# Kernel tuning notes

Measured on AMD Instinct MI355X. Metric: run time of the kernel, lower is better.

The kernel has to match this reference:

```python
import jax, jax.numpy as jnp
import numpy as np

B, S = 128, 512          # batch, padded expression length
D = 256                  # kos/identifier embedding dim (asserted equal)
KIND_D = 8               # token-kind embedding dim
EXPR_D = 512             # expression_encoding_dim
KOS_VOCAB = 256
KIND_VOCAB = 8
NUM_IDS = 8192
PAD_IDX = 0              # padding_idx -> zero embedding row
IDENTIFIER_KIND = 3
KOS_KINDS = (4, 5, 6)    # OPERATOR, SEPARATOR, KEYWORD


def setup_inputs() -> dict:
    key = jax.random.key(0)
    ks = jax.random.split(key, 8)
    token_type = jax.random.randint(ks[0], (B, S), 0, KIND_VOCAB, dtype=jnp.int32)
    kos_token_index = jax.random.randint(ks[1], (B * S,), 0, KOS_VOCAB, dtype=jnp.int32)
    identifier_indices = jax.random.randint(ks[2], (B * S,), 0, NUM_IDS, dtype=jnp.int32)
    encoded_identifiers = jax.random.normal(ks[3], (NUM_IDS, D), jnp.float32)
    kind_emb = jax.random.normal(ks[4], (KIND_VOCAB, KIND_D), jnp.float32).at[PAD_IDX].set(0.0)
    kos_emb = jax.random.normal(ks[5], (KOS_VOCAB, D), jnp.float32).at[PAD_IDX].set(0.0)
    sp = 1.0 / np.sqrt(KIND_D + D)
    W_proj = jax.random.uniform(ks[6], (KIND_D + D, EXPR_D), jnp.float32, -sp, sp)
    b_proj = jnp.zeros((EXPR_D,), jnp.float32)
    sa = 1.0 / np.sqrt(EXPR_D)
    W_add = jax.random.uniform(ks[7], (EXPR_D, EXPR_D), jnp.float32, -sa, sa)
    b_add = jnp.zeros((EXPR_D,), jnp.float32)
    return {
        'token_type': token_type,
        'kos_token_index': kos_token_index,
        'identifier_indices': identifier_indices,
        'encoded_identifiers': encoded_identifiers,
        'kind_emb': kind_emb,
        'kos_emb': kos_emb,
        'W_proj': W_proj,
        'b_proj': b_proj,
        'W_add': W_add,
        'b_add': b_add,
    }


def reference(token_type, kos_token_index, identifier_indices, encoded_identifiers,
              kind_emb, kos_emb, W_proj, b_proj, W_add, b_add):
    # token-kind embedding lookup: [B, S, KIND_D]
    kind_e = kind_emb[token_type]

    flat_kind = token_type.reshape(-1)                       # [B*S]
    is_id = flat_kind == IDENTIFIER_KIND
    is_kos = (flat_kind == KOS_KINDS[0]) | (flat_kind == KOS_KINDS[1]) | (flat_kind == KOS_KINDS[2])

    # embedding-table gathers (sources for masked_scatter, consumed in order)
    id_src = encoded_identifiers[identifier_indices]         # [B*S, D]
    kos_src = kos_emb[kos_token_index]                       # [B*S, D]

    # masked_scatter semantics: the k-th True position gets the k-th source row
    rank_id = jnp.maximum(jnp.cumsum(is_id) - 1, 0)
    rank_kos = jnp.maximum(jnp.cumsum(is_kos) - 1, 0)
    enc = jnp.where(is_id[:, None], id_src[rank_id], jnp.float32(0.0))
    enc = jnp.where(is_kos[:, None], kos_src[rank_kos], enc)
    enc = enc.reshape(B, S, D)

    # concat + 2-layer MLP (dropout is identity in eval mode)
    x = jnp.concatenate([kind_e, enc], axis=-1)              # [B, S, KIND_D + D]
    x = jax.nn.relu(x @ W_proj + b_proj)                     # [B, S, EXPR_D]
    x = jax.nn.relu(x @ W_add + b_add)                       # [B, S, EXPR_D]
    return x
```

## Files before the change

### kernel.cpp

```cpp
#include <hip/hip_runtime.h>
#include <hip/hip_bf16.h>

#define BB 128
#define SS 512
#define NPOS (BB*SS)
#define DD 256
#define KIND_D 8
#define EXPR_D 512
#define KOS_VOCAB 256
#define NUM_IDS 8192
#define IDENTIFIER_KIND 3
#define TROWS 9088

typedef unsigned short u16;
typedef __attribute__((ext_vector_type(8))) short s16x8;
typedef __attribute__((ext_vector_type(8))) unsigned short u16x8;
typedef __attribute__((ext_vector_type(4))) float f32x4;

__device__ __forceinline__ u16 bf16bits(float v) {
    __hip_bfloat16 h = __float2bfloat16(v);
    return *(u16*)&h;
}
__device__ __forceinline__ float bf16tof(u16 b) {
    __hip_bfloat16 h = *(__hip_bfloat16*)&b;
    return __bfloat162float(h);
}

__global__ __launch_bounds__(256) void prep_kernel(const float* __restrict__ W2,
                                                   const float* __restrict__ kind_emb,
                                                   const float* __restrict__ Wp,
                                                   const float* __restrict__ bp,
                                                   const int* __restrict__ token_type,
                                                   u16* __restrict__ Wt,
                                                   u16* __restrict__ Wt1,
                                                   float* __restrict__ kindc,
                                                   int2* __restrict__ blkcnt) {
    __shared__ float tile[32][33];
    __shared__ int swid[4], swkos[4];
    const int bi = blockIdx.x;
    const int t = threadIdx.x;

    if (bi < 256) {
        const int n0 = (bi & 15) * 32;
        const int k0 = (bi >> 4) * 32;
        const int lj = t & 31, li = t >> 5;
        #pragma unroll
        for (int p = 0; p < 4; ++p) {
            int i = li + p * 8;
            tile[i][lj] = W2[(size_t)(k0 + i) * EXPR_D + n0 + lj];
        }
        __syncthreads();
        #pragma unroll
        for (int p = 0; p < 4; ++p) {
            int j = li + p * 8;
            Wt[(size_t)(n0 + j) * EXPR_D + k0 + lj] = bf16bits(tile[lj][j]);
        }
    } else if (bi == 256) {
        #pragma unroll
        for (int rep = 0; rep < 2; ++rep) {
            int j = t + rep * 256;
            float bias = bp[j];
            for (int kind = 0; kind < 8; ++kind) {
                float a = bias;
                #pragma unroll
                for (int d = 0; d < KIND_D; ++d)
                    a = fmaf(kind_emb[kind * KIND_D + d], Wp[d * EXPR_D + j], a);
                kindc[kind * EXPR_D + j] = a;
            }
        }
    } else if (bi < 385) {
        const int idx = bi - 257;
        const int n0 = (idx & 15) * 32;
        const int k0 = (idx >> 4) * 32;
        const float* W1p = Wp + (size_t)KIND_D * EXPR_D;
        const int lj = t & 31, li = t >> 5;
        #pragma unroll
        for (int p = 0; p < 4; ++p) {
            int i = li + p * 8;
            tile[i][lj] = W1p[(size_t)(k0 + i) * EXPR_D + n0 + lj];
        }
        __syncthreads();
        #pragma unroll
        for (int p = 0; p < 4; ++p) {
            int j = li + p * 8;
            Wt1[(size_t)(n0 + j) * DD + k0 + lj] = bf16bits(tile[lj][j]);
        }
    } else {
        const int blk = bi - 385;
        const int lane = t & 63, wave = t >> 6;
        int k = token_type[blk * 256 + t];
        unsigned long long mid  = __ballot(k == IDENTIFIER_KIND);
        unsigned long long mkos = __ballot(k >= 4 && k <= 6);
        if (lane == 0) { swid[wave] = __popcll(mid); swkos[wave] = __popcll(mkos); }
        __syncthreads();
        if (t == 0) {
            int a = 0, c = 0;
            #pragma unroll
            for (int w = 0; w < 4; ++w) { a += swid[w]; c += swkos[w]; }
            blkcnt[blk] = make_int2(a, c);
        }
    }
}

__global__ __launch_bounds__(256) void scatter_kernel(const int* __restrict__ token_type,
                                                      const int2* __restrict__ blkcnt,
                                                      const int* __restrict__ kos_idx,
                                                      const int* __restrict__ id_idx,
                                                      int* __restrict__ sel2) {
    __shared__ int2 sbase;
    __shared__ int swid[4], swkos[4];
    const int b = blockIdx.x, t = threadIdx.x;
    const int lane = t & 63, wave = t >> 6;
    if (t < 64) {
        int a = 0, c = 0;
        for (int i = t; i < b; i += 64) { int2 v = blkcnt[i]; a += v.x; c += v.y; }
        #pragma unroll
        for (int off = 32; off; off >>= 1) { a += __shfl_down(a, off); c += __shfl_down(c, off); }
        if (t == 0) sbase = make_int2(a, c);
    }
    const int idx = b * 256 + t;
    const int k = token_type[idx];
    const bool fid  = (k == IDENTIFIER_KIND);
    const bool fkos = (k >= 4 && k <= 6);
    unsigned long long mid  = __ballot(fid);
    unsigned long long mkos = __ballot(fkos);
    if (lane == 0) { swid[wave] = __popcll(mid); swkos[wave] = __popcll(mkos); }
    __syncthreads();
    int bid = 0, bkos = 0;
    for (int w = 0; w < wave; ++w) { bid += swid[w]; bkos += swkos[w]; }
    unsigned long long below = (1ull << lane) - 1ull;
    int s;
    if (fid)       s = id_idx[sbase.x + bid + __popcll(mid & below)];
    else if (fkos) s = 8192 + (k - 4) * 256 + kos_idx[sbase.y + bkos + __popcll(mkos & below)];
    else           s = 8960 + k;
    sel2[idx] = s;
}

__global__ __launch_bounds__(512, 2) void table_kernel(const float* __restrict__ enc_ids,
                                                       const float* __restrict__ kos_emb,
                                                       const u16* __restrict__ Wt1,
                                                       const float* __restrict__ kindc,
                                                       u16* __restrict__ Thi) {
    __shared__ u16 sAhi[2][128 * 64];
    __shared__ u16 sAlo[2][128 * 64];
    __shared__ u16 sB[2][256 * 64];

    const int t = threadIdx.x;
    const int row0 = blockIdx.x * 128;
    const int col0 = blockIdx.y * 256;

    const int ar = t >> 2;
    const int ac = (t & 3) * 16;
    const int br = t >> 1;
    const int bc = (t & 1) * 32;

    const int arow = row0 + ar;
    const float* Arow;
    bool hasrc = true;
    if (arow < NUM_IDS)        Arow = &enc_ids[(size_t)arow * DD];
    else if (arow < 8960)      Arow = &kos_emb[(size_t)((arow - NUM_IDS) & 255) * DD];
    else { Arow = enc_ids; hasrc = false; }
    const u16* Brow = &Wt1[(size_t)(col0 + br) * DD];

    const int lane = t & 63;
    const int wid  = t >> 6;
    const int wr = wid >> 2, wc = wid & 3;
    const int lrow = lane & 15, lkg = lane >> 4;

    f32x4 acc[4][4];
    #pragma unroll
    for (int mi = 0; mi < 4; ++mi)
        #pragma unroll
        for (int ni = 0; ni < 4; ++ni)
            acc[mi][ni] = (f32x4){0.f, 0.f, 0.f, 0.f};

    f32x4 av[4];
    u16x8 bv[4];

    auto STAGE_ISSUE = [&](int kc) {
        const int kb = kc * 64;
        #pragma unroll
        for (int j = 0; j < 4; ++j)
            av[j] = hasrc ? *(const f32x4*)&Arow[kb + ac + j * 4] : (f32x4){0.f,0.f,0.f,0.f};
        #pragma unroll
        for (int j = 0; j < 4; ++j) bv[j] = *(const u16x8*)&Brow[kb + bc + j * 8];
    };

    auto WRITE = [&](int buf) {
        u16 hi[16], lo[16];
        #pragma unroll
        for (int j = 0; j < 4; ++j)
            #pragma unroll
            for (int e = 0; e < 4; ++e) {
                float r = av[j][e];
                u16 h = bf16bits(r);
                hi[j * 4 + e] = h;
                lo[j * 4 + e] = bf16bits(r - bf16tof(h));
            }
        const int abase = ar * 128;
        const int o0 = abase + ((ac * 2) ^ ((ar & 7) << 4));
        const int o1 = abase + ((ac * 2 + 16) ^ ((ar & 7) << 4));
        *(u16x8*)((char*)sAhi[buf] + o0) = *(const u16x8*)&hi[0];
        *(u16x8*)((char*)sAhi[buf] + o1) = *(const u16x8*)&hi[8];
        *(u16x8*)((char*)sAlo[buf] + o0) = *(const u16x8*)&lo[0];
        *(u16x8*)((char*)sAlo[buf] + o1) = *(const u16x8*)&lo[8];
        const int bbase = br * 128;
        #pragma unroll
        for (int j = 0; j < 4; ++j) {
            int off = bbase + ((bc * 2 + j * 16) ^ ((br & 7) << 4));
            *(u16x8*)((char*)sB[buf] + off) = bv[j];
        }
    };

    auto COMPUTE = [&](int buf) {
        #pragma unroll
        for (int ks = 0; ks < 2; ++ks) {
            s16x8 ah[4], al[4], bbf[4];
            #pragma unroll
            for (int mi = 0; mi < 4; ++mi) {
                int row = wr * 64 + mi * 16 + lrow;
                int off = row * 128 + ((ks * 64 + lkg * 16) ^ ((row & 7) << 4));
                ah[mi] = *(const s16x8*)((const char*)sAhi[buf] + off);
                al[mi] = *(const s16x8*)((const char*)sAlo[buf] + off);
            }
            #pragma unroll
            for (int ni = 0; ni < 4; ++ni) {
                int row = wc * 64 + ni * 16 + lrow;
                int off = row * 128 + ((ks * 64 + lkg * 16) ^ ((row & 7) << 4));
                bbf[ni] = *(const s16x8*)((const char*)sB[buf] + off);
            }
            #pragma unroll
            for (int mi = 0; mi < 4; ++mi)
                #pragma unroll
                for (int ni = 0; ni < 4; ++ni) {
                    acc[mi][ni] = __builtin_amdgcn_mfma_f32_16x16x32_bf16(ah[mi], bbf[ni], acc[mi][ni], 0, 0, 0);
                    acc[mi][ni] = __builtin_amdgcn_mfma_f32_16x16x32_bf16(al[mi], bbf[ni], acc[mi][ni], 0, 0, 0);
                }
        }
    };

    STAGE_ISSUE(0);
    WRITE(0);
    __syncthreads();
    int cur = 0;
    #pragma unroll 1
    for (int kc = 0; kc < 4; ++kc) {
        if (kc < 3) STAGE_ISSUE(kc + 1);
        COMPUTE(cur);
        if (kc < 3) WRITE(cur ^ 1);
        __syncthreads();
        cur ^= 1;
    }

    #pragma unroll
    for (int ni = 0; ni < 4; ++ni) {
        int col = col0 + wc * 64 + ni * 16 + lrow;
        #pragma unroll
        for (int mi = 0; mi < 4; ++mi) {
            int rbase = row0 + wr * 64 + mi * 16 + lkg * 4;
            #pragma unroll
            for (int j = 0; j < 4; ++j) {
                int rg = rbase + j;
                int kind = (rg < NUM_IDS) ? 3
                         : (rg < 8960) ? 4 + ((rg - NUM_IDS) >> 8)
                         : (rg < 8968) ? (rg - 8960) : 0;
                float v = acc[mi][ni][j] + kindc[kind * EXPR_D + col];
                Thi[(size_t)rg * EXPR_D + col] = bf16bits(fmaxf(v, 0.f));
            }
        }
    }
}

__global__ __launch_bounds__(512, 4) void table2_kernel(const u16* __restrict__ Thi,
                                                        const u16* __restrict__ Wt,
                                                        const float* __restrict__ b2,
                                                        float* __restrict__ O) {
    __shared__ u16 sA[2][128 * 32];
    __shared__ u16 sB[2][256 * 32];

    const int t = threadIdx.x;
    const int row0 = blockIdx.x * 128;
    const int col0 = blockIdx.y * 256;

    const int ar = t >> 2;
    const int ac8 = (t & 3) * 8;
    const int br = t >> 1;
    const int bc16 = (t & 1) * 16;

    const u16* Arow = &Thi[(size_t)(row0 + ar) * EXPR_D + ac8];
    const u16* Brow = &Wt[(size_t)(col0 + br) * EXPR_D + bc16];

    const int lane = t & 63;
    const int wid  = t >> 6;
    const int wr = wid >> 2, wc = wid & 3;
    const int lrow = lane & 15, lkg = lane >> 4;

    f32x4 acc[4][4];
    #pragma unroll
    for (int mi = 0; mi < 4; ++mi)
        #pragma unroll
        for (int ni = 0; ni < 4; ++ni)
            acc[mi][ni] = (f32x4){0.f, 0.f, 0.f, 0.f};

    u16x8 av;
    u16x8 bv[2];

    auto STAGE_ISSUE = [&](int kc) {
        const int kb = kc * 32;
        av = *(const u16x8*)&Arow[kb];
        bv[0] = *(const u16x8*)&Brow[kb];
        bv[1] = *(const u16x8*)&Brow[kb + 8];
    };

    auto WRITE = [&](int buf) {
        int aoff = ar * 64 + ((ac8 * 2) ^ ((ar & 3) << 4));
        *(u16x8*)((char*)sA[buf] + aoff) = av;
        #pragma unroll
        for (int j = 0; j < 2; ++j) {
            int boff = br * 64 + ((bc16 * 2 + j * 16) ^ ((br & 3) << 4));
            *(u16x8*)((char*)sB[buf] + boff) = bv[j];
        }
    };

    auto COMPUTE = [&](int buf) {
        s16x8 a[4], b[4];
        #pragma unroll
        for (int mi = 0; mi < 4; ++mi) {
            int row = wr * 64 + mi * 16 + lrow;
            int off = row * 64 + ((lkg * 16) ^ ((row & 3) << 4));
            a[mi] = *(const s16x8*)((const char*)sA[buf] + off);
        }
        #pragma unroll
        for (int ni = 0; ni < 4; ++ni) {
            int row = wc * 64 + ni * 16 + lrow;
            int off = row * 64 + ((lkg * 16) ^ ((row & 3) << 4));
            b[ni] = *(const s16x8*)((const char*)sB[buf] + off);
        }
        #pragma unroll
        for (int mi = 0; mi < 4; ++mi)
            #pragma unroll
            for (int ni = 0; ni < 4; ++ni)
                acc[mi][ni] = __builtin_amdgcn_mfma_f32_16x16x32_bf16(a[mi], b[ni], acc[mi][ni], 0, 0, 0);
    };

    STAGE_ISSUE(0);
    WRITE(0);
    __syncthreads();
    int cur = 0;
    #pragma unroll 1
    for (int kc = 0; kc < 16; ++kc) {
        if (kc < 15) STAGE_ISSUE(kc + 1);
        COMPUTE(cur);
        if (kc < 15) WRITE(cur ^ 1);
        __syncthreads();
        cur ^= 1;
    }

    #pragma unroll
    for (int ni = 0; ni < 4; ++ni) {
        int col = col0 + wc * 64 + ni * 16 + lrow;
        float bias = b2[col];
        #pragma unroll
        for (int mi = 0; mi < 4; ++mi) {
            int rbase = row0 + wr * 64 + mi * 16 + lkg * 4;
            #pragma unroll
            for (int j = 0; j < 4; ++j)
                O[(size_t)(rbase + j) * EXPR_D + col] = fmaxf(acc[mi][ni][j] + bias, 0.f);
        }
    }
}

__global__ __launch_bounds__(256) void gather_kernel(const int* __restrict__ sel2,
                                                     const float* __restrict__ O,
                                                     float* __restrict__ out) {
    const int t = threadIdx.x;
    const int lane = t & 63, wave = t >> 6;
    const int base = blockIdx.x * 16;
    int rows[4];
    #pragma unroll
    for (int i = 0; i < 4; ++i) rows[i] = sel2[base + i * 4 + wave];
    #pragma unroll
    for (int i = 0; i < 4; ++i) {
        const int pos = base + i * 4 + wave;
        const f32x4* src = (const f32x4*)&O[(size_t)rows[i] * EXPR_D];
        f32x4* dst = (f32x4*)&out[(size_t)pos * EXPR_D];
        f32x4 v0 = src[lane];
        f32x4 v1 = src[lane + 64];
        __builtin_nontemporal_store(v0, &dst[lane]);
        __builtin_nontemporal_store(v1, &dst[lane + 64]);
    }
}

extern "C" void kernel_launch(void* const* d_in, const int* in_sizes, int n_in,
                              void* d_out, int out_size, void* d_ws, size_t ws_size,
                              hipStream_t stream) {
    const int*   token_type = (const int*)d_in[0];
    const int*   kos_idx    = (const int*)d_in[1];
    const int*   id_idx     = (const int*)d_in[2];
    const float* enc_ids    = (const float*)d_in[3];
    const float* kind_emb   = (const float*)d_in[4];
    const float* kos_emb    = (const float*)d_in[5];
    const float* Wp         = (const float*)d_in[6];
    const float* bp         = (const float*)d_in[7];
    const float* W2         = (const float*)d_in[8];
    const float* b2         = (const float*)d_in[9];
    float* out = (float*)d_out;

    char* ws = (char*)d_ws;
    int*   sel2   = (int*)ws;
    float* kindc  = (float*)(ws + 262144);
    int2*  blkcnt = (int2*)(ws + 278528);
    u16*   Wt     = (u16*)(ws + 282624);
    u16*   Wt1    = (u16*)(ws + 806912);
    u16*   Thi    = (u16*)(ws + 1069056);
    float* O      = (float*)(ws + 10375168);

    hipLaunchKernelGGL(prep_kernel, dim3(641), dim3(256), 0, stream,
                       W2, kind_emb, Wp, bp, token_type, Wt, Wt1, kindc, blkcnt);
    hipLaunchKernelGGL(scatter_kernel, dim3(256), dim3(256), 0, stream,
                       token_type, blkcnt, kos_idx, id_idx, sel2);
    hipLaunchKernelGGL(table_kernel, dim3(TROWS / 128, EXPR_D / 256), dim3(512), 0, stream,
                       enc_ids, kos_emb, Wt1, kindc, Thi);
    hipLaunchKernelGGL(table2_kernel, dim3(TROWS / 128, EXPR_D / 256), dim3(512), 0, stream,
                       Thi, Wt, b2, O);
    hipLaunchKernelGGL(gather_kernel, dim3(NPOS / 16), dim3(256), 0, stream,
                       sel2, O, out);
}
```

Baseline: 75.85 us.

## Fuse scatter into gather kernel and retile table GEMMs to 128x128 blocks

Removes the separate scatter kernel by computing masked-scatter row selection inside the gather kernel, where it is held in shared memory and never goes through global memory. The gather now runs 256 blocks, each copying 256 output rows. The two table GEMM kernels are retiled from 128x256 tiles with 512 threads to 128x128 tiles with 256 threads, which doubles the grid. The second GEMM also now uses a 64-wide K step instead of 32. The aim is to cut one launch and the sel2 round trip and to spread the GEMMs over more CUs, at the cost of fewer gather blocks and possibly lower per-block reuse.

```diff
diff --git a/kernel.cpp b/kernel.cpp
--- a/kernel.cpp
+++ b/kernel.cpp
@@ -102,15 +102,254 @@
     }
 }
 
-__global__ __launch_bounds__(256) void scatter_kernel(const int* __restrict__ token_type,
-                                                      const int2* __restrict__ blkcnt,
-                                                      const int* __restrict__ kos_idx,
-                                                      const int* __restrict__ id_idx,
-                                                      int* __restrict__ sel2) {
+__global__ __launch_bounds__(256) void table_kernel(const float* __restrict__ enc_ids,
+                                                    const float* __restrict__ kos_emb,
+                                                    const u16* __restrict__ Wt1,
+                                                    const float* __restrict__ kindc,
+                                                    u16* __restrict__ Thi) {
+    __shared__ u16 sAhi[2][128 * 64];
+    __shared__ u16 sAlo[2][128 * 64];
+    __shared__ u16 sB[2][128 * 64];
+
+    const int t = threadIdx.x;
+    const int row0 = blockIdx.x * 128;
+    const int col0 = blockIdx.y * 128;
+
+    const int ar = t >> 1;
+    const int ac = (t & 1) * 32;
+    const int br = ar, bc = ac;
+
+    const int arow = row0 + ar;
+    const float* Arow;
+    bool hasrc = true;
+    if (arow < NUM_IDS)        Arow = &enc_ids[(size_t)arow * DD];
+    else if (arow < 8960)      Arow = &kos_emb[(size_t)((arow - NUM_IDS) & 255) * DD];
+    else { Arow = enc_ids; hasrc = false; }
+    const u16* Brow = &Wt1[(size_t)(col0 + br) * DD];
+
+    const int lane = t & 63;
+    const int wid  = t >> 6;
+    const int wr = wid >> 1, wc = wid & 1;
+    const int lrow = lane & 15, lkg = lane >> 4;
+
+    f32x4 acc[4][4];
+    #pragma unroll
+    for (int mi = 0; mi < 4; ++mi)
+        #pragma unroll
+        for (int ni = 0; ni < 4; ++ni)
+            acc[mi][ni] = (f32x4){0.f, 0.f, 0.f, 0.f};
+
+    f32x4 av[8];
+    u16x8 bv[4];
+
+    auto STAGE_ISSUE = [&](int kc) {
+        const int kb = kc * 64;
+        #pragma unroll
+        for (int j = 0; j < 8; ++j)
+            av[j] = hasrc ? *(const f32x4*)&Arow[kb + ac + j * 4] : (f32x4){0.f,0.f,0.f,0.f};
+        #pragma unroll
+        for (int j = 0; j < 4; ++j) bv[j] = *(const u16x8*)&Brow[kb + bc + j * 8];
+    };
+
+    auto WRITE = [&](int buf) {
+        u16 hi[32], lo[32];
+        #pragma unroll
+        for (int j = 0; j < 8; ++j)
+            #pragma unroll
+            for (int e = 0; e < 4; ++e) {
+                float r = av[j][e];
+                u16 h = bf16bits(r);
+                hi[j * 4 + e] = h;
+                lo[j * 4 + e] = bf16bits(r - bf16tof(h));
+            }
+        const int abase = ar * 128;
+        #pragma unroll
+        for (int j = 0; j < 4; ++j) {
+            int off = abase + ((ac * 2 + j * 16) ^ ((ar & 7) << 4));
+            *(u16x8*)((char*)sAhi[buf] + off) = *(const u16x8*)&hi[j * 8];
+            *(u16x8*)((char*)sAlo[buf] + off) = *(const u16x8*)&lo[j * 8];
+        }
+        const int bbase = br * 128;
+        #pragma unroll
+        for (int j = 0; j < 4; ++j) {
+            int off = bbase + ((bc * 2 + j * 16) ^ ((br & 7) << 4));
+            *(u16x8*)((char*)sB[buf] + off) = bv[j];
+        }
+    };
+
+    auto COMPUTE = [&](int buf) {
+        #pragma unroll
+        for (int ks = 0; ks < 2; ++ks) {
+            s16x8 ah[4], al[4], bbf[4];
+            #pragma unroll
+            for (int mi = 0; mi < 4; ++mi) {
+                int row = wr * 64 + mi * 16 + lrow;
+                int off = row * 128 + ((ks * 64 + lkg * 16) ^ ((row & 7) << 4));
+                ah[mi] = *(const s16x8*)((const char*)sAhi[buf] + off);
+                al[mi] = *(const s16x8*)((const char*)sAlo[buf] + off);
+            }
+            #pragma unroll
+            for (int ni = 0; ni < 4; ++ni) {
+                int row = wc * 64 + ni * 16 + lrow;
+                int off = row * 128 + ((ks * 64 + lkg * 16) ^ ((row & 7) << 4));
+                bbf[ni] = *(const s16x8*)((const char*)sB[buf] + off);
+            }
+            #pragma unroll
+            for (int mi = 0; mi < 4; ++mi)
+                #pragma unroll
+                for (int ni = 0; ni < 4; ++ni) {
+                    acc[mi][ni] = __builtin_amdgcn_mfma_f32_16x16x32_bf16(ah[mi], bbf[ni], acc[mi][ni], 0, 0, 0);
+                    acc[mi][ni] = __builtin_amdgcn_mfma_f32_16x16x32_bf16(al[mi], bbf[ni], acc[mi][ni], 0, 0, 0);
+                }
+        }
+    };
+
+    STAGE_ISSUE(0);
+    WRITE(0);
+    __syncthreads();
+    int cur = 0;
+    #pragma unroll 1
+    for (int kc = 0; kc < 4; ++kc) {
+        if (kc < 3) STAGE_ISSUE(kc + 1);
+        COMPUTE(cur);
+        if (kc < 3) WRITE(cur ^ 1);
+        __syncthreads();
+        cur ^= 1;
+    }
+
+    #pragma unroll
+    for (int ni = 0; ni < 4; ++ni) {
+        int col = col0 + wc * 64 + ni * 16 + lrow;
+        #pragma unroll
+        for (int mi = 0; mi < 4; ++mi) {
+            int rbase = row0 + wr * 64 + mi * 16 + lkg * 4;
+            #pragma unroll
+            for (int j = 0; j < 4; ++j) {
+                int rg = rbase + j;
+                int kind = (rg < NUM_IDS) ? 3
+                         : (rg < 8960) ? 4 + ((rg - NUM_IDS) >> 8)
+                         : (rg < 8968) ? (rg - 8960) : 0;
+                float v = acc[mi][ni][j] + kindc[kind * EXPR_D + col];
+                Thi[(size_t)rg * EXPR_D + col] = bf16bits(fmaxf(v, 0.f));
+            }
+        }
+    }
+}
+
+__global__ __launch_bounds__(256, 2) void table2_kernel(const u16* __restrict__ Thi,
+                                                        const u16* __restrict__ Wt,
+                                                        const float* __restrict__ b2,
+                                                        float* __restrict__ O) {
+    __shared__ u16 sA[2][128 * 64];
+    __shared__ u16 sB[2][128 * 64];
+
+    const int t = threadIdx.x;
+    const int row0 = blockIdx.x * 128;
+    const int col0 = blockIdx.y * 128;
+
+    const int ar = t >> 1;
+    const int ac = (t & 1) * 32;
+    const int br = ar, bc = ac;
+
+    const u16* Arow = &Thi[(size_t)(row0 + ar) * EXPR_D];
+    const u16* Brow = &Wt[(size_t)(col0 + br) * EXPR_D];
+
+    const int lane = t & 63;
+    const int wid  = t >> 6;
+    const int wr = wid >> 1, wc = wid & 1;
+    const int lrow = lane & 15, lkg = lane >> 4;
+
+    f32x4 acc[4][4];
+    #pragma unroll
+    for (int mi = 0; mi < 4; ++mi)
+        #pragma unroll
+        for (int ni = 0; ni < 4; ++ni)
+            acc[mi][ni] = (f32x4){0.f, 0.f, 0.f, 0.f};
+
+    u16x8 av[4], bv[4];
+
+    auto STAGE_ISSUE = [&](int kc) {
+        const int kb = kc * 64;
+        #pragma unroll
+        for (int j = 0; j < 4; ++j) {
+            av[j] = *(const u16x8*)&Arow[kb + ac + j * 8];
+            bv[j] = *(const u16x8*)&Brow[kb + bc + j * 8];
+        }
+    };
+
+    auto WRITE = [&](int buf) {
+        const int abase = ar * 128;
+        #pragma unroll
+        for (int j = 0; j < 4; ++j) {
+            int off = abase + ((ac * 2 + j * 16) ^ ((ar & 7) << 4));
+            *(u16x8*)((char*)sA[buf] + off) = av[j];
+            *(u16x8*)((char*)sB[buf] + off) = bv[j];
+        }
+    };
+
+    auto COMPUTE = [&](int buf) {
+        #pragma unroll
+        for (int ks = 0; ks < 2; ++ks) {
+            s16x8 a[4], b[4];
+            #pragma unroll
+            for (int mi = 0; mi < 4; ++mi) {
+                int row = wr * 64 + mi * 16 + lrow;
+                int off = row * 128 + ((ks * 64 + lkg * 16) ^ ((row & 7) << 4));
+                a[mi] = *(const s16x8*)((const char*)sA[buf] + off);
+            }
+            #pragma unroll
+            for (int ni = 0; ni < 4; ++ni) {
+                int row = wc * 64 + ni * 16 + lrow;
+                int off = row * 128 + ((ks * 64 + lkg * 16) ^ ((row & 7) << 4));
+                b[ni] = *(const s16x8*)((const char*)sB[buf] + off);
+            }
+            #pragma unroll
+            for (int mi = 0; mi < 4; ++mi)
+                #pragma unroll
+                for (int ni = 0; ni < 4; ++ni)
+                    acc[mi][ni] = __builtin_amdgcn_mfma_f32_16x16x32_bf16(a[mi], b[ni], acc[mi][ni], 0, 0, 0);
+        }
+    };
+
+    STAGE_ISSUE(0);
+    WRITE(0);
+    __syncthreads();
+    int cur = 0;
+    #pragma unroll 1
+    for (int kc = 0; kc < 8; ++kc) {
+        if (kc < 7) STAGE_ISSUE(kc + 1);
+        COMPUTE(cur);
+        if (kc < 7) WRITE(cur ^ 1);
+        __syncthreads();
+        cur ^= 1;
+    }
+
+    #pragma unroll
+    for (int ni = 0; ni < 4; ++ni) {
+        int col = col0 + wc * 64 + ni * 16 + lrow;
+        float bias = b2[col];
+        #pragma unroll
+        for (int mi = 0; mi < 4; ++mi) {
+            int rbase = row0 + wr * 64 + mi * 16 + lkg * 4;
+            #pragma unroll
+            for (int j = 0; j < 4; ++j)
+                O[(size_t)(rbase + j) * EXPR_D + col] = fmaxf(acc[mi][ni][j] + bias, 0.f);
+        }
+    }
+}
+
+__global__ __launch_bounds__(256) void gather_kernel(const int* __restrict__ token_type,
+                                                     const int2* __restrict__ blkcnt,
+                                                     const int* __restrict__ kos_idx,
+                                                     const int* __restrict__ id_idx,
+                                                     const float* __restrict__ O,
+                                                     float* __restrict__ out) {
+    __shared__ int srow[256];
+    __shared__ int swid[4], swkos[4];
     __shared__ int2 sbase;
-    __shared__ int swid[4], swkos[4];
     const int b = blockIdx.x, t = threadIdx.x;
     const int lane = t & 63, wave = t >> 6;
+
     if (t < 64) {
         int a = 0, c = 0;
         for (int i = t; i < b; i += 64) { int2 v = blkcnt[i]; a += v.x; c += v.y; }
@@ -133,257 +372,14 @@
     if (fid)       s = id_idx[sbase.x + bid + __popcll(mid & below)];
     else if (fkos) s = 8192 + (k - 4) * 256 + kos_idx[sbase.y + bkos + __popcll(mkos & below)];
     else           s = 8960 + k;
-    sel2[idx] = s;
-}
-
-__global__ __launch_bounds__(512, 2) void table_kernel(const float* __restrict__ enc_ids,
-                                                       const float* __restrict__ kos_emb,
-                                                       const u16* __restrict__ Wt1,
-                                                       const float* __restrict__ kindc,
-                                                       u16* __restrict__ Thi) {
-    __shared__ u16 sAhi[2][128 * 64];
-    __shared__ u16 sAlo[2][128 * 64];
-    __shared__ u16 sB[2][256 * 64];
-
-    const int t = threadIdx.x;
-    const int row0 = blockIdx.x * 128;
-    const int col0 = blockIdx.y * 256;
-
-    const int ar = t >> 2;
-    const int ac = (t & 3) * 16;
-    const int br = t >> 1;
-    const int bc = (t & 1) * 32;
-
-    const int arow = row0 + ar;
-    const float* Arow;
-    bool hasrc = true;
-    if (arow < NUM_IDS)        Arow = &enc_ids[(size_t)arow * DD];
-    else if (arow < 8960)      Arow = &kos_emb[(size_t)((arow - NUM_IDS) & 255) * DD];
-    else { Arow = enc_ids; hasrc = false; }
-    const u16* Brow = &Wt1[(size_t)(col0 + br) * DD];
-
-    const int lane = t & 63;
-    const int wid  = t >> 6;
-    const int wr = wid >> 2, wc = wid & 3;
-    const int lrow = lane & 15, lkg = lane >> 4;
-
-    f32x4 acc[4][4];
-    #pragma unroll
-    for (int mi = 0; mi < 4; ++mi)
-        #pragma unroll
-        for (int ni = 0; ni < 4; ++ni)
-            acc[mi][ni] = (f32x4){0.f, 0.f, 0.f, 0.f};
-
-    f32x4 av[4];
-    u16x8 bv[4];
-
-    auto STAGE_ISSUE = [&](int kc) {
-        const int kb = kc * 64;
-        #pragma unroll
-        for (int j = 0; j < 4; ++j)
-            av[j] = hasrc ? *(const f32x4*)&Arow[kb + ac + j * 4] : (f32x4){0.f,0.f,0.f,0.f};
-        #pragma unroll
-        for (int j = 0; j < 4; ++j) bv[j] = *(const u16x8*)&Brow[kb + bc + j * 8];
-    };
-
-    auto WRITE = [&](int buf) {
-        u16 hi[16], lo[16];
-        #pragma unroll
-        for (int j = 0; j < 4; ++j)
-            #pragma unroll
-            for (int e = 0; e < 4; ++e) {
-                float r = av[j][e];
-                u16 h = bf16bits(r);
-                hi[j * 4 + e] = h;
-                lo[j * 4 + e] = bf16bits(r - bf16tof(h));
-            }
-        const int abase = ar * 128;
-        const int o0 = abase + ((ac * 2) ^ ((ar & 7) << 4));
-        const int o1 = abase + ((ac * 2 + 16) ^ ((ar & 7) << 4));
-        *(u16x8*)((char*)sAhi[buf] + o0) = *(const u16x8*)&hi[0];
-        *(u16x8*)((char*)sAhi[buf] + o1) = *(const u16x8*)&hi[8];
-        *(u16x8*)((char*)sAlo[buf] + o0) = *(const u16x8*)&lo[0];
-        *(u16x8*)((char*)sAlo[buf] + o1) = *(const u16x8*)&lo[8];
-        const int bbase = br * 128;
-        #pragma unroll
-        for (int j = 0; j < 4; ++j) {
-            int off = bbase + ((bc * 2 + j * 16) ^ ((br & 7) << 4));
-            *(u16x8*)((char*)sB[buf] + off) = bv[j];
-        }
-    };
-
-    auto COMPUTE = [&](int buf) {
-        #pragma unroll
-        for (int ks = 0; ks < 2; ++ks) {
-            s16x8 ah[4], al[4], bbf[4];
-            #pragma unroll
-            for (int mi = 0; mi < 4; ++mi) {
-                int row = wr * 64 + mi * 16 + lrow;
-                int off = row * 128 + ((ks * 64 + lkg * 16) ^ ((row & 7) << 4));
-                ah[mi] = *(const s16x8*)((const char*)sAhi[buf] + off);
-                al[mi] = *(const s16x8*)((const char*)sAlo[buf] + off);
-            }
-            #pragma unroll
-            for (int ni = 0; ni < 4; ++ni) {
-                int row = wc * 64 + ni * 16 + lrow;
-                int off = row * 128 + ((ks * 64 + lkg * 16) ^ ((row & 7) << 4));
-                bbf[ni] = *(const s16x8*)((const char*)sB[buf] + off);
-            }
-            #pragma unroll
-            for (int mi = 0; mi < 4; ++mi)
-                #pragma unroll
-                for (int ni = 0; ni < 4; ++ni) {
-                    acc[mi][ni] = __builtin_amdgcn_mfma_f32_16x16x32_bf16(ah[mi], bbf[ni], acc[mi][ni], 0, 0, 0);
-                    acc[mi][ni] = __builtin_amdgcn_mfma_f32_16x16x32_bf16(al[mi], bbf[ni], acc[mi][ni], 0, 0, 0);
-                }
-        }
-    };
-
-    STAGE_ISSUE(0);
-    WRITE(0);
+    srow[t] = s;
     __syncthreads();
-    int cur = 0;
+
     #pragma unroll 1
-    for (int kc = 0; kc < 4; ++kc) {
-        if (kc < 3) STAGE_ISSUE(kc + 1);
-        COMPUTE(cur);
-        if (kc < 3) WRITE(cur ^ 1);
-        __syncthreads();
-        cur ^= 1;
-    }
-
-    #pragma unroll
-    for (int ni = 0; ni < 4; ++ni) {
-        int col = col0 + wc * 64 + ni * 16 + lrow;
-        #pragma unroll
-        for (int mi = 0; mi < 4; ++mi) {
-            int rbase = row0 + wr * 64 + mi * 16 + lkg * 4;
-            #pragma unroll
-            for (int j = 0; j < 4; ++j) {
-                int rg = rbase + j;
-                int kind = (rg < NUM_IDS) ? 3
-                         : (rg < 8960) ? 4 + ((rg - NUM_IDS) >> 8)
-                         : (rg < 8968) ? (rg - 8960) : 0;
-                float v = acc[mi][ni][j] + kindc[kind * EXPR_D + col];
-                Thi[(size_t)rg * EXPR_D + col] = bf16bits(fmaxf(v, 0.f));
-            }
-        }
-    }
-}
-
-__global__ __launch_bounds__(512, 4) void table2_kernel(const u16* __restrict__ Thi,
-                                                        const u16* __restrict__ Wt,
-                                                        const float* __restrict__ b2,
-                                                        float* __restrict__ O) {
-    __shared__ u16 sA[2][128 * 32];
-    __shared__ u16 sB[2][256 * 32];
-
-    const int t = threadIdx.x;
-    const int row0 = blockIdx.x * 128;
-    const int col0 = blockIdx.y * 256;
-
-    const int ar = t >> 2;
-    const int ac8 = (t & 3) * 8;
-    const int br = t >> 1;
-    const int bc16 = (t & 1) * 16;
-
-    const u16* Arow = &Thi[(size_t)(row0 + ar) * EXPR_D + ac8];
-    const u16* Brow = &Wt[(size_t)(col0 + br) * EXPR_D + bc16];
-
-    const int lane = t & 63;
-    const int wid  = t >> 6;
-    const int wr = wid >> 2, wc = wid & 3;
-    const int lrow = lane & 15, lkg = lane >> 4;
-
-    f32x4 acc[4][4];
-    #pragma unroll
-    for (int mi = 0; mi < 4; ++mi)
-        #pragma unroll
-        for (int ni = 0; ni < 4; ++ni)
-            acc[mi][ni] = (f32x4){0.f, 0.f, 0.f, 0.f};
-
-    u16x8 av;
-    u16x8 bv[2];
-
-    auto STAGE_ISSUE = [&](int kc) {
-        const int kb = kc * 32;
-        av = *(const u16x8*)&Arow[kb];
-        bv[0] = *(const u16x8*)&Brow[kb];
-        bv[1] = *(const u16x8*)&Brow[kb + 8];
-    };
-
-    auto WRITE = [&](int buf) {
-        int aoff = ar * 64 + ((ac8 * 2) ^ ((ar & 3) << 4));
-        *(u16x8*)((char*)sA[buf] + aoff) = av;
-        #pragma unroll
-        for (int j = 0; j < 2; ++j) {
-            int boff = br * 64 + ((bc16 * 2 + j * 16) ^ ((br & 3) << 4));
-            *(u16x8*)((char*)sB[buf] + boff) = bv[j];
-        }
-    };
-
-    auto COMPUTE = [&](int buf) {
-        s16x8 a[4], b[4];
-        #pragma unroll
-        for (int mi = 0; mi < 4; ++mi) {
-            int row = wr * 64 + mi * 16 + lrow;
-            int off = row * 64 + ((lkg * 16) ^ ((row & 3) << 4));
-            a[mi] = *(const s16x8*)((const char*)sA[buf] + off);
-        }
-        #pragma unroll
-        for (int ni = 0; ni < 4; ++ni) {
-            int row = wc * 64 + ni * 16 + lrow;
-            int off = row * 64 + ((lkg * 16) ^ ((row & 3) << 4));
-            b[ni] = *(const s16x8*)((const char*)sB[buf] + off);
-        }
-        #pragma unroll
-        for (int mi = 0; mi < 4; ++mi)
-            #pragma unroll
-            for (int ni = 0; ni < 4; ++ni)
-                acc[mi][ni] = __builtin_amdgcn_mfma_f32_16x16x32_bf16(a[mi], b[ni], acc[mi][ni], 0, 0, 0);
-    };
-
-    STAGE_ISSUE(0);
-    WRITE(0);
-    __syncthreads();
-    int cur = 0;
-    #pragma unroll 1
-    for (int kc = 0; kc < 16; ++kc) {
-        if (kc < 15) STAGE_ISSUE(kc + 1);
-        COMPUTE(cur);
-        if (kc < 15) WRITE(cur ^ 1);
-        __syncthreads();
-        cur ^= 1;
-    }
-
-    #pragma unroll
-    for (int ni = 0; ni < 4; ++ni) {
-        int col = col0 + wc * 64 + ni * 16 + lrow;
-        float bias = b2[col];
-        #pragma unroll
-        for (int mi = 0; mi < 4; ++mi) {
-            int rbase = row0 + wr * 64 + mi * 16 + lkg * 4;
-            #pragma unroll
-            for (int j = 0; j < 4; ++j)
-                O[(size_t)(rbase + j) * EXPR_D + col] = fmaxf(acc[mi][ni][j] + bias, 0.f);
-        }
-    }
-}
-
-__global__ __launch_bounds__(256) void gather_kernel(const int* __restrict__ sel2,
-                                                     const float* __restrict__ O,
-                                                     float* __restrict__ out) {
-    const int t = threadIdx.x;
-    const int lane = t & 63, wave = t >> 6;
-    const int base = blockIdx.x * 16;
-    int rows[4];
-    #pragma unroll
-    for (int i = 0; i < 4; ++i) rows[i] = sel2[base + i * 4 + wave];
-    #pragma unroll
-    for (int i = 0; i < 4; ++i) {
-        const int pos = base + i * 4 + wave;
-        const f32x4* src = (const f32x4*)&O[(size_t)rows[i] * EXPR_D];
-        f32x4* dst = (f32x4*)&out[(size_t)pos * EXPR_D];
+    for (int i = wave; i < 256; i += 4) {
+        const int row = srow[i];
+        const f32x4* src = (const f32x4*)&O[(size_t)row * EXPR_D];
+        f32x4* dst = (f32x4*)&out[((size_t)b * 256 + i) * EXPR_D];
         f32x4 v0 = src[lane];
         f32x4 v1 = src[lane + 64];
         __builtin_nontemporal_store(v0, &dst[lane]);
@@ -407,22 +403,19 @@
     float* out = (float*)d_out;
 
     char* ws = (char*)d_ws;
-    int*   sel2   = (int*)ws;
-    float* kindc  = (float*)(ws + 262144);
-    int2*  blkcnt = (int2*)(ws + 278528);
-    u16*   Wt     = (u16*)(ws + 282624);
-    u16*   Wt1    = (u16*)(ws + 806912);
-    u16*   Thi    = (u16*)(ws + 1069056);
-    float* O      = (float*)(ws + 10375168);
+    float* kindc  = (float*)(ws);
+    int2*  blkcnt = (int2*)(ws + 16384);
+    u16*   Wt     = (u16*)(ws + 20480);
+    u16*   Wt1    = (u16*)(ws + 544768);
+    u16*   Thi    = (u16*)(ws + 806912);
+    float* O      = (float*)(ws + 10113024);
 
     hipLaunchKernelGGL(prep_kernel, dim3(641), dim3(256), 0, stream,
                        W2, kind_emb, Wp, bp, token_type, Wt, Wt1, kindc, blkcnt);
-    hipLaunchKernelGGL(scatter_kernel, dim3(256), dim3(256), 0, stream,
-                       token_type, blkcnt, kos_idx, id_idx, sel2);
-    hipLaunchKernelGGL(table_kernel, dim3(TROWS / 128, EXPR_D / 256), dim3(512), 0, stream,
+    hipLaunchKernelGGL(table_kernel, dim3(TROWS / 128, EXPR_D / 128), dim3(256), 0, stream,
                        enc_ids, kos_emb, Wt1, kindc, Thi);
-    hipLaunchKernelGGL(table2_kernel, dim3(TROWS / 128, EXPR_D / 256), dim3(512), 0, stream,
+    hipLaunchKernelGGL(table2_kernel, dim3(TROWS / 128, EXPR_D / 128), dim3(256), 0, stream,
                        Thi, Wt, b2, O);
-    hipLaunchKernelGGL(gather_kernel, dim3(NPOS / 16), dim3(256), 0, stream,
-                       sel2, O, out);
-}
+    hipLaunchKernelGGL(gather_kernel, dim3(256), dim3(256), 0, stream,
+                       token_type, blkcnt, kos_idx, id_idx, O, out);
+}
```

Measured after the change: 89.42 us. 17.9% more time.
